# Performance work log

Hardware: AMD Instinct MI355X
Metric: run time of the kernel (lower is better)

The kernel has to match this reference:

```python
import jax, jax.numpy as jnp
import numpy as np

SIGMAS = [15, 80, 250]  # hardcoded defaults in retinex_MSR


def _gauss_k1d(sigma):
    # matches get_gauss_kernel(sigma, dim=1)
    ksize = int(np.floor(sigma * 6) / 2) * 2 + 1
    k = np.arange(ksize, dtype=np.float32) - ksize // 2
    k = np.exp(-k ** 2 / (2.0 * sigma ** 2))
    k /= k.sum()
    return jnp.asarray(k)


def _gauss_blur(x, k1d):
    # x: (N, 1, H, W); separable blur with zero padding, same as F.conv2d
    K = k1d.shape[0]
    pad = K // 2
    dn = ('NCHW', 'OIHW', 'NCHW')
    kv = k1d.reshape(1, 1, K, 1)
    kh = k1d.reshape(1, 1, 1, K)
    x = jax.lax.conv_general_dilated(x, kv, (1, 1), [(pad, pad), (0, 0)], dimension_numbers=dn)
    x = jax.lax.conv_general_dilated(x, kh, (1, 1), [(0, 0), (pad, pad)], dimension_numbers=dn)
    return x


def setup_inputs() -> dict:
    key = jax.random.key(0)
    img = jax.random.uniform(key, (16, 3, 512, 512), dtype=jnp.float32)
    return {"img": img}


def reference(img):
    B, C, H, W = img.shape
    # all channels processed identically as single-channel depthwise convs:
    # fold channels into batch for one big conv per sigma
    x = img.astype(jnp.float32).reshape(B * C, 1, H, W)
    w = 1.0 / len(SIGMAS)  # default equal weights summing to 1
    r = jnp.zeros((B * C, 1, H, W), dtype=jnp.float32)
    for sigma in SIGMAS:
        r = r + jnp.log(_gauss_blur(x, _gauss_k1d(sigma)) + 1.0) * w
    r = r.reshape(B, C, H, W)
    # per-channel min-max stretch, global over batch and spatial dims
    mmin = r.min(axis=(0, 2, 3), keepdims=True)
    mmax = r.max(axis=(0, 2, 3), keepdims=True)
    return (r - mmin) / (mmax - mmin)
```

## Files before the change

### kernel.cpp

```cpp
#include <hip/hip_runtime.h>
#include <math.h>


#define NSL 48

#define W0_OFF 0
#define W1_OFF 512
#define W2_OFF 1280
#define MM_OFF 2816
#define G16_BYTE_OFF 16384
#define X16_BYTE_OFF 1589248
#define T16_BYTE_OFF 26755072

typedef _Float16 half8 __attribute__((ext_vector_type(8)));
typedef _Float16 half4v __attribute__((ext_vector_type(4)));
typedef float f32x4 __attribute__((ext_vector_type(4)));

__device__ __forceinline__ void gload16(const void* g, void* l) {
  __builtin_amdgcn_global_load_lds(
      (const __attribute__((address_space(1))) void*)g,
      (__attribute__((address_space(3))) void*)l, 16, 0, 0);
}

__global__ void wkern(float* __restrict__ ws) {
  __shared__ float red[256];
  const int s = blockIdx.x;
  const int Ks[3] = {91, 481, 1501};
  const float sg[3] = {15.f, 80.f, 250.f};
  const int off[3] = {W0_OFF, W1_OFF, W2_OFF};
  const int alloc[3] = {512, 768, 1536};
  const int K = Ks[s], A = alloc[s];
  float* wb = ws + off[s];
  const int t = threadIdx.x;
  for (int i = t; i < A; i += 256) wb[i] = 0.f;
  __syncthreads();
  const float inv2s2 = 1.f / (2.f * sg[s] * sg[s]);
  float part = 0.f;
  for (int i = t; i < K; i += 256) {
    const float d = (float)(i - K / 2);
    const float e = __expf(-d * d * inv2s2);
    wb[16 + i] = e;
    part += e;
  }
  red[t] = part;
  __syncthreads();
  for (int st = 128; st > 0; st >>= 1) {
    if (t < st) red[t] += red[t + st];
    __syncthreads();
  }
  const float inv = 1.f / red[0];
  for (int i = t; i < K; i += 256) wb[16 + i] *= inv;
}

__global__ void mm_init(unsigned* __restrict__ mm) {
  const int t = threadIdx.x;
  if (t < 3) mm[t] = 0xFFFFFFFFu;
  else if (t < 6) mm[t] = 0u;
}

__global__ void gkern(const float* __restrict__ ws, _Float16* __restrict__ gb) {
  const int y = blockIdx.x;
  const int s = blockIdx.y;
  const int Rs[3] = {45, 240, 750};
  const int off[3] = {W0_OFF, W1_OFF, W2_OFF};
  const float* w = ws + off[s] + 16;
  _Float16* g = gb + ((size_t)s << 18) + ((size_t)y << 9);
  const int R = Rs[s], K = 2 * R + 1;
  for (int x = threadIdx.x; x < 512; x += 256) {
    const int i = x - y + R;
    const float v = (i >= 0 && i < K) ? w[i] : 0.f;
    g[x] = (_Float16)v;
  }
}

__global__ __launch_bounds__(256) void xconv(const float* __restrict__ X,
                                             _Float16* __restrict__ X16) {
  const size_t i = ((size_t)blockIdx.x * 256 + threadIdx.x) << 3;
  const float4 v0 = *reinterpret_cast<const float4*>(X + i);
  const float4 v1 = *reinterpret_cast<const float4*>(X + i + 4);
  half8 h;
  h[0] = (_Float16)v0.x; h[1] = (_Float16)v0.y;
  h[2] = (_Float16)v0.z; h[3] = (_Float16)v0.w;
  h[4] = (_Float16)v1.x; h[5] = (_Float16)v1.y;
  h[6] = (_Float16)v1.z; h[7] = (_Float16)v1.w;
  *reinterpret_cast<half8*>(X16 + i) = h;
}

__global__ __launch_bounds__(256) void gemm1_k(const _Float16* __restrict__ X16,
                                               const _Float16* __restrict__ G16,
                                               _Float16* __restrict__ T16) {
  __shared__ __align__(16) _Float16 As[128 * 32];
  __shared__ __align__(16) _Float16 Bs[128 * 32];
  const int t = threadIdx.x;
  const int lane = t & 63, wave = t >> 6;
  const int wr = wave >> 1, wc = wave & 1;
  const int lr = lane & 15, lg = lane >> 4;
  const int bn = blockIdx.x << 7;
  const int bm = blockIdx.y << 7;
  const int z = blockIdx.z;
  const int s = z / NSL;
  const int slice = z - s * NSL;
  const int Rs[3] = {45, 240, 750};
  const int R = Rs[s];
  const _Float16* Xp = X16 + ((size_t)slice << 18);
  const _Float16* G = G16 + ((size_t)s << 18);
  _Float16* Tout = T16 + (size_t)s * ((size_t)NSL << 18) + ((size_t)slice << 18);

  int klo = bn - R;
  klo = (klo > 0 ? klo : 0) >> 5;
  int khi = bn + 127 + R;
  if (khi > 511) khi = 511;
  khi >>= 5;

  f32x4 acc[4][4];
#pragma unroll
  for (int i = 0; i < 4; ++i)
#pragma unroll
    for (int j = 0; j < 4; ++j) acc[i][j] = (f32x4){0.f, 0.f, 0.f, 0.f};

  for (int kt = klo; kt <= khi; ++kt) {
    const int k0 = kt << 5;
    __syncthreads();
#pragma unroll
    for (int q = 0; q < 2; ++q) {
      const int idx = (q << 8) + t;
      const int row = idx >> 2;
      const int c8 = (idx & 3) << 3;
      gload16(Xp + ((size_t)(bm + row) << 9) + k0 + c8, &As[idx << 3]);
      gload16(G + ((size_t)(bn + row) << 9) + k0 + c8, &Bs[idx << 3]);
    }
    __syncthreads();

    half8 af[4], bf[4];
#pragma unroll
    for (int f = 0; f < 4; ++f) {
      af[f] = *reinterpret_cast<const half8*>(
          &As[(((wr << 6) + (f << 4) + lr) << 5) + (lg << 3)]);
      bf[f] = *reinterpret_cast<const half8*>(
          &Bs[(((wc << 6) + (f << 4) + lr) << 5) + (lg << 3)]);
    }
#pragma unroll
    for (int fm = 0; fm < 4; ++fm)
#pragma unroll
      for (int fn = 0; fn < 4; ++fn)
        acc[fm][fn] = __builtin_amdgcn_mfma_f32_16x16x32_f16(af[fm], bf[fn],
                                                             acc[fm][fn], 0, 0, 0);
  }

#pragma unroll
  for (int fm = 0; fm < 4; ++fm)
#pragma unroll
    for (int fn = 0; fn < 4; ++fn) {
      const int n = bn + (wc << 6) + (fn << 4) + lr;
      const int rb = bm + (wr << 6) + (fm << 4) + (lg << 2);
      half4v h;
      h[0] = (_Float16)acc[fm][fn][0];
      h[1] = (_Float16)acc[fm][fn][1];
      h[2] = (_Float16)acc[fm][fn][2];
      h[3] = (_Float16)acc[fm][fn][3];
      *reinterpret_cast<half4v*>(&Tout[((size_t)n << 9) + rb]) = h;
    }
}

__global__ __launch_bounds__(256) void gemm2_k(const _Float16* __restrict__ G16,
                                               const _Float16* __restrict__ T16,
                                               float* __restrict__ out,
                                               unsigned* __restrict__ mm) {
  __shared__ __align__(16) _Float16 As[128 * 32];
  __shared__ __align__(16) _Float16 Bs[128 * 32];
  __shared__ float smn[4], smx[4];
  const int t = threadIdx.x;
  const int lane = t & 63, wave = t >> 6;
  const int wr = wave >> 1, wc = wave & 1;
  const int lr = lane & 15, lg = lane >> 4;
  const int bn = blockIdx.x << 7;
  const int bm = blockIdx.y << 7;
  const int slice = blockIdx.z;
  const float w3 = 1.f / 3.f;
  const int Rs[3] = {45, 240, 750};

  f32x4 res[4][4];
#pragma unroll
  for (int i = 0; i < 4; ++i)
#pragma unroll
    for (int j = 0; j < 4; ++j) res[i][j] = (f32x4){0.f, 0.f, 0.f, 0.f};

#pragma unroll 1
  for (int s = 0; s < 3; ++s) {
    const int R = Rs[s];
    const _Float16* G = G16 + ((size_t)s << 18);
    const _Float16* T = T16 + (size_t)s * ((size_t)NSL << 18) + ((size_t)slice << 18);
    int klo = bm - R;
    klo = (klo > 0 ? klo : 0) >> 5;
    int khi = bm + 127 + R;
    if (khi > 511) khi = 511;
    khi >>= 5;

    f32x4 acc[4][4];
#pragma unroll
    for (int i = 0; i < 4; ++i)
#pragma unroll
      for (int j = 0; j < 4; ++j) acc[i][j] = (f32x4){0.f, 0.f, 0.f, 0.f};

    for (int kt = klo; kt <= khi; ++kt) {
      const int k0 = kt << 5;
      __syncthreads();
#pragma unroll
      for (int q = 0; q < 2; ++q) {
        const int idx = (q << 8) + t;
        const int row = idx >> 2;
        const int c8 = (idx & 3) << 3;
        gload16(G + ((size_t)(bm + row) << 9) + k0 + c8, &As[idx << 3]);
        gload16(T + ((size_t)(bn + row) << 9) + k0 + c8, &Bs[idx << 3]);
      }
      __syncthreads();

      half8 af[4], bf[4];
#pragma unroll
      for (int f = 0; f < 4; ++f) {
        af[f] = *reinterpret_cast<const half8*>(
            &As[(((wr << 6) + (f << 4) + lr) << 5) + (lg << 3)]);
        bf[f] = *reinterpret_cast<const half8*>(
            &Bs[(((wc << 6) + (f << 4) + lr) << 5) + (lg << 3)]);
      }
#pragma unroll
      for (int fm = 0; fm < 4; ++fm)
#pragma unroll
        for (int fn = 0; fn < 4; ++fn)
          acc[fm][fn] = __builtin_amdgcn_mfma_f32_16x16x32_f16(af[fm], bf[fn],
                                                               acc[fm][fn], 0, 0, 0);
    }

#pragma unroll
    for (int fm = 0; fm < 4; ++fm)
#pragma unroll
      for (int fn = 0; fn < 4; ++fn)
#pragma unroll
        for (int j = 0; j < 4; ++j)
          res[fm][fn][j] += w3 * __logf(acc[fm][fn][j] + 1.f);
  }

  float mn = 3.4e38f, mx = -3.4e38f;
#pragma unroll
  for (int fm = 0; fm < 4; ++fm)
#pragma unroll
    for (int fn = 0; fn < 4; ++fn) {
      const int rb = bm + (wr << 6) + (fm << 4) + (lg << 2);
      const int cg = bn + (wc << 6) + (fn << 4) + lr;
      float* op = out + ((size_t)slice << 18) + ((size_t)rb << 9) + cg;
#pragma unroll
      for (int j = 0; j < 4; ++j) {
        const float v = res[fm][fn][j];
        op[j << 9] = v;
        mn = fminf(mn, v);
        mx = fmaxf(mx, v);
      }
    }
#pragma unroll
  for (int off = 32; off > 0; off >>= 1) {
    mn = fminf(mn, __shfl_xor(mn, off));
    mx = fmaxf(mx, __shfl_xor(mx, off));
  }
  if (lane == 0) {
    smn[wave] = mn;
    smx[wave] = mx;
  }
  __syncthreads();
  if (t == 0) {
    mn = fminf(fminf(smn[0], smn[1]), fminf(smn[2], smn[3]));
    mx = fmaxf(fmaxf(smx[0], smx[1]), fmaxf(smx[2], smx[3]));
    const int ch = slice % 3;
    atomicMin(&mm[ch], __float_as_uint(mn));
    atomicMax(&mm[3 + ch], __float_as_uint(mx));
  }
}

__global__ __launch_bounds__(256) void norm_k(float* __restrict__ r,
                                              const unsigned* __restrict__ mm) {
  const int b = blockIdx.x;
  const int slice = b >> 4;
  const int piece = b & 15;
  const int ch = slice % 3;
  const float mn = __uint_as_float(mm[ch]);
  const float mx = __uint_as_float(mm[3 + ch]);
  const float inv = 1.f / (mx - mn);
  float* p = r + ((size_t)slice << 18) + (piece << 14);
  const int t = threadIdx.x;
  for (int q = 0; q < 16; ++q) {
    float4 v = *reinterpret_cast<const float4*>(&p[(q * 256 + t) << 2]);
    v.x = (v.x - mn) * inv;
    v.y = (v.y - mn) * inv;
    v.z = (v.z - mn) * inv;
    v.w = (v.w - mn) * inv;
    *reinterpret_cast<float4*>(&p[(q * 256 + t) << 2]) = v;
  }
}

extern "C" void kernel_launch(void* const* d_in, const int* in_sizes, int n_in,
                              void* d_out, int out_size, void* d_ws, size_t ws_size,
                              hipStream_t stream) {
  const float* img = (const float*)d_in[0];
  float* out = (float*)d_out;
  float* wsf = (float*)d_ws;
  unsigned* mm = (unsigned*)(wsf + MM_OFF);
  _Float16* G16 = (_Float16*)((char*)d_ws + G16_BYTE_OFF);
  _Float16* X16 = (_Float16*)((char*)d_ws + X16_BYTE_OFF);
  _Float16* T16 = (_Float16*)((char*)d_ws + T16_BYTE_OFF);

  wkern<<<3, 256, 0, stream>>>(wsf);
  mm_init<<<1, 64, 0, stream>>>(mm);
  gkern<<<dim3(512, 3), 256, 0, stream>>>(wsf, G16);
  xconv<<<6144, 256, 0, stream>>>(img, X16);

  gemm1_k<<<dim3(4, 4, 3 * NSL), 256, 0, stream>>>(X16, G16, T16);
  gemm2_k<<<dim3(4, 4, NSL), 256, 0, stream>>>(G16, T16, out, mm);

  norm_k<<<768, 256, 0, stream>>>(out, mm);
}
```

Measured before the change: 179.8 us.

## Double-buffer LDS tiles in both GEMMs and swap gemm1 operand roles

Both banded GEMM kernels now use two LDS buffers so the next K-tile's global-to-LDS load is issued before the current tile's MFMAs run, with one barrier per iteration instead of two. This is meant to hide global load latency behind compute. gemm1 also swaps operands (G as A, X as B), so the band limits follow the row tile and the intermediate is written row-major with scalar half stores instead of transposed half4 stores. That change risks less efficient uncoalesced stores, and the doubled LDS footprint may lower occupancy.

```diff
diff --git a/kernel.cpp b/kernel.cpp
--- a/kernel.cpp
+++ b/kernel.cpp
@@ -13,7 +13,6 @@
 #define T16_BYTE_OFF 26755072
 
 typedef _Float16 half8 __attribute__((ext_vector_type(8)));
-typedef _Float16 half4v __attribute__((ext_vector_type(4)));
 typedef float f32x4 __attribute__((ext_vector_type(4)));
 
 __device__ __forceinline__ void gload16(const void* g, void* l) {
@@ -86,11 +85,37 @@
   *reinterpret_cast<half8*>(X16 + i) = h;
 }
 
+#define STAGE(buf, k0)                                                              \
+  do {                                                                              \
+    _Pragma("unroll") for (int q = 0; q < 2; ++q) {                                 \
+      const int idx = (q << 8) + t;                                                 \
+      const int row = idx >> 2;                                                     \
+      const int c8 = (idx & 3) << 3;                                                \
+      gload16(Ap + ((size_t)(bm + row) << 9) + (k0) + c8, &As[buf][idx << 3]);      \
+      gload16(Bp + ((size_t)(bn + row) << 9) + (k0) + c8, &Bs[buf][idx << 3]);      \
+    }                                                                               \
+  } while (0)
+
+#define FRAGS_AND_MFMA(buf)                                                         \
+  do {                                                                              \
+    half8 af[4], bf[4];                                                             \
+    _Pragma("unroll") for (int f = 0; f < 4; ++f) {                                 \
+      af[f] = *reinterpret_cast<const half8*>(                                      \
+          &As[buf][(((wr << 6) + (f << 4) + lr) << 5) + (lg << 3)]);                \
+      bf[f] = *reinterpret_cast<const half8*>(                                      \
+          &Bs[buf][(((wc << 6) + (f << 4) + lr) << 5) + (lg << 3)]);                \
+    }                                                                               \
+    _Pragma("unroll") for (int fm = 0; fm < 4; ++fm)                                \
+        _Pragma("unroll") for (int fn = 0; fn < 4; ++fn)                            \
+        acc[fm][fn] = __builtin_amdgcn_mfma_f32_16x16x32_f16(af[fm], bf[fn],        \
+                                                             acc[fm][fn], 0, 0, 0); \
+  } while (0)
+
 __global__ __launch_bounds__(256) void gemm1_k(const _Float16* __restrict__ X16,
                                                const _Float16* __restrict__ G16,
                                                _Float16* __restrict__ T16) {
-  __shared__ __align__(16) _Float16 As[128 * 32];
-  __shared__ __align__(16) _Float16 Bs[128 * 32];
+  __shared__ __align__(16) _Float16 As[2][128 * 32];
+  __shared__ __align__(16) _Float16 Bs[2][128 * 32];
   const int t = threadIdx.x;
   const int lane = t & 63, wave = t >> 6;
   const int wr = wave >> 1, wc = wave & 1;
@@ -102,13 +127,13 @@
   const int slice = z - s * NSL;
   const int Rs[3] = {45, 240, 750};
   const int R = Rs[s];
-  const _Float16* Xp = X16 + ((size_t)slice << 18);
-  const _Float16* G = G16 + ((size_t)s << 18);
-  _Float16* Tout = T16 + (size_t)s * ((size_t)NSL << 18) + ((size_t)slice << 18);
-
-  int klo = bn - R;
+  const _Float16* Ap = G16 + ((size_t)s << 18);
+  const _Float16* Bp = X16 + ((size_t)slice << 18);
+  _Float16* Tout = T16 + ((size_t)z << 18);
+
+  int klo = bm - R;
   klo = (klo > 0 ? klo : 0) >> 5;
-  int khi = bn + 127 + R;
+  int khi = bm + 127 + R;
   if (khi > 511) khi = 511;
   khi >>= 5;
 
@@ -118,47 +143,25 @@
 #pragma unroll
     for (int j = 0; j < 4; ++j) acc[i][j] = (f32x4){0.f, 0.f, 0.f, 0.f};
 
+  int cur = 0;
+  STAGE(0, klo << 5);
+  __syncthreads();
   for (int kt = klo; kt <= khi; ++kt) {
-    const int k0 = kt << 5;
+    if (kt < khi) STAGE(cur ^ 1, (kt + 1) << 5);
+    FRAGS_AND_MFMA(cur);
     __syncthreads();
-#pragma unroll
-    for (int q = 0; q < 2; ++q) {
-      const int idx = (q << 8) + t;
-      const int row = idx >> 2;
-      const int c8 = (idx & 3) << 3;
-      gload16(Xp + ((size_t)(bm + row) << 9) + k0 + c8, &As[idx << 3]);
-      gload16(G + ((size_t)(bn + row) << 9) + k0 + c8, &Bs[idx << 3]);
-    }
-    __syncthreads();
-
-    half8 af[4], bf[4];
-#pragma unroll
-    for (int f = 0; f < 4; ++f) {
-      af[f] = *reinterpret_cast<const half8*>(
-          &As[(((wr << 6) + (f << 4) + lr) << 5) + (lg << 3)]);
-      bf[f] = *reinterpret_cast<const half8*>(
-          &Bs[(((wc << 6) + (f << 4) + lr) << 5) + (lg << 3)]);
-    }
-#pragma unroll
-    for (int fm = 0; fm < 4; ++fm)
-#pragma unroll
-      for (int fn = 0; fn < 4; ++fn)
-        acc[fm][fn] = __builtin_amdgcn_mfma_f32_16x16x32_f16(af[fm], bf[fn],
-                                                             acc[fm][fn], 0, 0, 0);
+    cur ^= 1;
   }
 
 #pragma unroll
   for (int fm = 0; fm < 4; ++fm)
 #pragma unroll
     for (int fn = 0; fn < 4; ++fn) {
-      const int n = bn + (wc << 6) + (fn << 4) + lr;
-      const int rb = bm + (wr << 6) + (fm << 4) + (lg << 2);
-      half4v h;
-      h[0] = (_Float16)acc[fm][fn][0];
-      h[1] = (_Float16)acc[fm][fn][1];
-      h[2] = (_Float16)acc[fm][fn][2];
-      h[3] = (_Float16)acc[fm][fn][3];
-      *reinterpret_cast<half4v*>(&Tout[((size_t)n << 9) + rb]) = h;
+      const int a0 = bm + (wr << 6) + (fm << 4) + (lg << 2);
+      const int b0 = bn + (wc << 6) + (fn << 4) + lr;
+#pragma unroll
+      for (int j = 0; j < 4; ++j)
+        Tout[((size_t)(a0 + j) << 9) + b0] = (_Float16)acc[fm][fn][j];
     }
 }
 
@@ -166,8 +169,8 @@
                                                const _Float16* __restrict__ T16,
                                                float* __restrict__ out,
                                                unsigned* __restrict__ mm) {
-  __shared__ __align__(16) _Float16 As[128 * 32];
-  __shared__ __align__(16) _Float16 Bs[128 * 32];
+  __shared__ __align__(16) _Float16 As[2][128 * 32];
+  __shared__ __align__(16) _Float16 Bs[2][128 * 32];
   __shared__ float smn[4], smx[4];
   const int t = threadIdx.x;
   const int lane = t & 63, wave = t >> 6;
@@ -185,11 +188,12 @@
 #pragma unroll
     for (int j = 0; j < 4; ++j) res[i][j] = (f32x4){0.f, 0.f, 0.f, 0.f};
 
+  int cur = 0;
 #pragma unroll 1
   for (int s = 0; s < 3; ++s) {
     const int R = Rs[s];
-    const _Float16* G = G16 + ((size_t)s << 18);
-    const _Float16* T = T16 + (size_t)s * ((size_t)NSL << 18) + ((size_t)slice << 18);
+    const _Float16* Ap = G16 + ((size_t)s << 18);
+    const _Float16* Bp = T16 + ((size_t)(s * NSL + slice) << 18);
     int klo = bm - R;
     klo = (klo > 0 ? klo : 0) >> 5;
     int khi = bm + 127 + R;
@@ -202,33 +206,13 @@
 #pragma unroll
       for (int j = 0; j < 4; ++j) acc[i][j] = (f32x4){0.f, 0.f, 0.f, 0.f};
 
+    STAGE(cur, klo << 5);
+    __syncthreads();
     for (int kt = klo; kt <= khi; ++kt) {
-      const int k0 = kt << 5;
+      if (kt < khi) STAGE(cur ^ 1, (kt + 1) << 5);
+      FRAGS_AND_MFMA(cur);
       __syncthreads();
-#pragma unroll
-      for (int q = 0; q < 2; ++q) {
-        const int idx = (q << 8) + t;
-        const int row = idx >> 2;
-        const int c8 = (idx & 3) << 3;
-        gload16(G + ((size_t)(bm + row) << 9) + k0 + c8, &As[idx << 3]);
-        gload16(T + ((size_t)(bn + row) << 9) + k0 + c8, &Bs[idx << 3]);
-      }
-      __syncthreads();
-
-      half8 af[4], bf[4];
-#pragma unroll
-      for (int f = 0; f < 4; ++f) {
-        af[f] = *reinterpret_cast<const half8*>(
-            &As[(((wr << 6) + (f << 4) + lr) << 5) + (lg << 3)]);
-        bf[f] = *reinterpret_cast<const half8*>(
-            &Bs[(((wc << 6) + (f << 4) + lr) << 5) + (lg << 3)]);
-      }
-#pragma unroll
-      for (int fm = 0; fm < 4; ++fm)
-#pragma unroll
-        for (int fn = 0; fn < 4; ++fn)
-          acc[fm][fn] = __builtin_amdgcn_mfma_f32_16x16x32_f16(af[fm], bf[fn],
-                                                               acc[fm][fn], 0, 0, 0);
+      cur ^= 1;
     }
 
 #pragma unroll
```

After: 163.2 us. -9.2%, faster.
